# Optimization experiments

Measured on AMD Instinct MI355X. Metric: run time of the kernel, lower is better.

Reference implementation:

```python
import jax, jax.numpy as jnp
import numpy as np

B, T, H, NH = 2, 2048, 2048, 16
HD = H // NH  # 128


def setup_inputs() -> dict:
    key = jax.random.key(0)
    ks = jax.random.split(key, 7)
    s = 1.0 / np.sqrt(H)
    return {
        "x": jax.random.normal(ks[0], (B, T, H), jnp.float32),
        "cos": jax.random.uniform(ks[1], (1, 1, T, HD), jnp.float32),
        "sin": jax.random.uniform(ks[2], (1, 1, T, HD), jnp.float32),
        "Wq": jax.random.normal(ks[3], (H, H), jnp.float32) * s,
        "Wk": jax.random.normal(ks[4], (H, H), jnp.float32) * s,
        "Wv": jax.random.normal(ks[5], (H, H), jnp.float32) * s,
        "Wo": jax.random.normal(ks[6], (H, H), jnp.float32) * s,
    }


def rotate_half(x):
    d = x.shape[-1] // 2
    return jnp.concatenate([-x[..., d:], x[..., :d]], axis=-1)


def reference(x, cos, sin, Wq, Wk, Wv, Wo):
    b, t, h = x.shape
    # torch Linear: y = x @ W.T; reshape to (B, NH, T, HD)
    def proj(W):
        return jnp.einsum('bth,oh->bto', x, W).reshape(b, t, NH, HD).transpose(0, 2, 1, 3)
    q, k, v = proj(Wq), proj(Wk), proj(Wv)
    q = q * cos + rotate_half(q) * sin
    k = k * cos + rotate_half(k) * sin
    scale = 1.0 / jnp.sqrt(jnp.asarray(HD, x.dtype))
    scores = jnp.einsum('bhqd,bhkd->bhqk', q, k) * scale  # [B,NH,T,T]
    causal = jnp.tril(jnp.ones((t, t), bool))
    scores = jnp.where(causal, scores, jnp.asarray(-jnp.inf, scores.dtype))
    attn = jax.nn.softmax(scores, axis=-1)
    out = jnp.einsum('bhqk,bhkd->bhqd', attn, v)  # [B,NH,T,HD]
    out = out.transpose(0, 2, 1, 3).reshape(b, t, h)
    return jnp.einsum('bth,oh->bto', out, Wo)
```

## Files before the change

### kernel.cpp

```cpp
#include <hip/hip_runtime.h>
#include <hip/hip_bf16.h>

#define B_  2
#define T_  2048
#define H_  2048
#define NH_ 16
#define HD_ 128
#define QKVN 6144

typedef __attribute__((ext_vector_type(8))) short  short8;
typedef __attribute__((ext_vector_type(4))) float  floatx4;

__device__ __forceinline__ unsigned short f2bf(float x) {
    union { float f; unsigned int u; } c; c.f = x;
    unsigned int r = c.u + 0x7FFF + ((c.u >> 16) & 1);
    return (unsigned short)(r >> 16);
}
__device__ __forceinline__ float bf2f(unsigned short u) {
    union { float f; unsigned int i; } c;
    c.i = ((unsigned int)u) << 16;
    return c.f;
}

__device__ __forceinline__ void gload_lds16(const void* g, void* l) {
    __builtin_amdgcn_global_load_lds(
        (__attribute__((address_space(1))) void*)g,
        (__attribute__((address_space(3))) void*)l, 16, 0, 0);
}

__global__ __launch_bounds__(256) void f32_to_bf16(
    const float* __restrict__ src, unsigned short* __restrict__ dst, int n)
{
    const int i = (blockIdx.x * 256 + threadIdx.x) * 4;
    if (i < n) {
        float4 v = *(const float4*)(src + i);
        ushort4 o;
        o.x = f2bf(v.x); o.y = f2bf(v.y); o.z = f2bf(v.z); o.w = f2bf(v.w);
        *(ushort4*)(dst + i) = o;
    }
}

template<bool BF16_OUT>
__global__ __launch_bounds__(512, 1) void gemm8(
    const unsigned short* __restrict__ A,
    const unsigned short* __restrict__ W,
    float* __restrict__ Yf, unsigned short* __restrict__ Yb,
    int M, int N, int K)
{
    __shared__ __attribute__((aligned(16))) unsigned short As[2][256 * 64];
    __shared__ __attribute__((aligned(16))) unsigned short Bs[2][256 * 64];

    const int tid  = threadIdx.x;
    const int lane = tid & 63;
    const int n16  = lane & 15;
    const int quad = lane >> 4;
    const int w    = tid >> 6;
    const int wm   = w >> 2;
    const int wn   = w & 3;

    const int m0 = blockIdx.y * 256;
    const int n0 = blockIdx.x * 256;

    const int r0  = tid >> 3;
    const int g0  = ((tid & 7) ^ (r0 & 7)) * 8;
    const int r1  = r0 + 64;
    const int g1  = ((tid & 7) ^ (r1 & 7)) * 8;
    const unsigned short* A0p = A + (size_t)(m0 + r0) * K + g0;
    const unsigned short* A1p = A + (size_t)(m0 + r1) * K + g1;
    const unsigned short* B0p = W + (size_t)(n0 + r0) * K + g0;
    const unsigned short* B1p = W + (size_t)(n0 + r1) * K + g1;
    const size_t hstep = (size_t)128 * K;

    floatx4 acc[8][4];
    #pragma unroll
    for (int i = 0; i < 8; i++)
        #pragma unroll
        for (int j = 0; j < 4; j++) acc[i][j] = (floatx4){0.f, 0.f, 0.f, 0.f};

    const int nt = K >> 6;

    gload_lds16(A0p,         &As[0][(size_t)tid * 8]);
    gload_lds16(A1p,         &As[0][(size_t)(tid + 512) * 8]);
    gload_lds16(A0p + hstep, &As[0][8192 + (size_t)tid * 8]);
    gload_lds16(A1p + hstep, &As[0][8192 + (size_t)(tid + 512) * 8]);
    gload_lds16(B0p,         &Bs[0][(size_t)tid * 8]);
    gload_lds16(B1p,         &Bs[0][(size_t)(tid + 512) * 8]);
    gload_lds16(B0p + hstep, &Bs[0][8192 + (size_t)tid * 8]);
    gload_lds16(B1p + hstep, &Bs[0][8192 + (size_t)(tid + 512) * 8]);

    for (int t = 0; t < nt; ++t) {
        const unsigned short* Ac = &As[t & 1][0];
        const unsigned short* Bc = &Bs[t & 1][0];
        unsigned short* An = &As[(t & 1) ^ 1][0];
        unsigned short* Bn = &Bs[(t & 1) ^ 1][0];
        const bool pre = (t + 1 < nt);
        const size_t knext = (size_t)(t + 1) << 6;

        short8 bfr[4][2];

        #pragma unroll
        for (int q = 0; q < 4; ++q) {
            short8 af[2][2];
            if (q == 0) {
                if (pre) {
                    gload_lds16(A0p + knext,         An + (size_t)tid * 8);
                    gload_lds16(A1p + knext,         An + (size_t)(tid + 512) * 8);
                    gload_lds16(A0p + knext + hstep, An + 8192 + (size_t)tid * 8);
                    gload_lds16(A1p + knext + hstep, An + 8192 + (size_t)(tid + 512) * 8);
                    asm volatile("s_waitcnt vmcnt(4)" ::: "memory");
                } else {
                    asm volatile("s_waitcnt vmcnt(0)" ::: "memory");
                }
                asm volatile("s_barrier" ::: "memory");
                #pragma unroll
                for (int j = 0; j < 2; ++j)
                    #pragma unroll
                    for (int ks = 0; ks < 2; ++ks)
                        af[j][ks] = *(const short8*)(Ac + (wm*128 + (q*2 + j)*16 + n16) * 64
                                                        + (((ks*4 + quad) ^ (n16 & 7)) * 8));
                #pragma unroll
                for (int ni = 0; ni < 4; ++ni)
                    #pragma unroll
                    for (int ks = 0; ks < 2; ++ks)
                        bfr[ni][ks] = *(const short8*)(Bc + (wn*64 + ni*16 + n16) * 64
                                                          + (((ks*4 + quad) ^ (n16 & 7)) * 8));
            } else {
                #pragma unroll
                for (int j = 0; j < 2; ++j)
                    #pragma unroll
                    for (int ks = 0; ks < 2; ++ks)
                        af[j][ks] = *(const short8*)(Ac + (wm*128 + (q*2 + j)*16 + n16) * 64
                                                        + (((ks*4 + quad) ^ (n16 & 7)) * 8));
                if (q == 1 && pre) {
                    gload_lds16(B0p + knext,         Bn + (size_t)tid * 8);
                    gload_lds16(B1p + knext,         Bn + (size_t)(tid + 512) * 8);
                    gload_lds16(B0p + knext + hstep, Bn + 8192 + (size_t)tid * 8);
                    gload_lds16(B1p + knext + hstep, Bn + 8192 + (size_t)(tid + 512) * 8);
                }
                asm volatile("s_barrier" ::: "memory");
            }
            asm volatile("s_waitcnt lgkmcnt(0)" ::: "memory");
            __builtin_amdgcn_sched_barrier(0);
            __builtin_amdgcn_s_setprio(1);
            #pragma unroll
            for (int ni = 0; ni < 4; ++ni)
                #pragma unroll
                for (int ks = 0; ks < 2; ++ks) {
                    acc[q*2+0][ni] = __builtin_amdgcn_mfma_f32_16x16x32_bf16(
                        af[0][ks], bfr[ni][ks], acc[q*2+0][ni], 0, 0, 0);
                    acc[q*2+1][ni] = __builtin_amdgcn_mfma_f32_16x16x32_bf16(
                        af[1][ks], bfr[ni][ks], acc[q*2+1][ni], 0, 0, 0);
                }
            __builtin_amdgcn_s_setprio(0);
            asm volatile("s_barrier" ::: "memory");
        }
    }

    #pragma unroll
    for (int mi = 0; mi < 8; ++mi) {
        const size_t rb = (size_t)(m0 + wm*128 + mi*16 + quad*4);
        #pragma unroll
        for (int r = 0; r < 4; ++r) {
            const size_t row = rb + r;
            #pragma unroll
            for (int ni = 0; ni < 4; ++ni) {
                const size_t col = n0 + wn*64 + ni*16 + n16;
                if (BF16_OUT) Yb[row * N + col] = f2bf(acc[mi][ni][r]);
                else          Yf[row * N + col] = acc[mi][ni][r];
            }
        }
    }
}

__global__ __launch_bounds__(256) void rope_convert_qk(
    const unsigned short* __restrict__ qkvp,
    const float* __restrict__ cosp, const float* __restrict__ sinp,
    unsigned short* __restrict__ qh, unsigned short* __restrict__ kh)
{
    const int idx  = blockIdx.x * 256 + threadIdx.x;
    const int d    = idx & 63;
    const int rest = idx >> 6;
    const int h    = rest & 15;
    const int bt   = rest >> 4;
    const int t    = bt & (T_ - 1);
    const int b    = bt >> 11;
    const size_t ibase = (size_t)bt * QKVN + h * HD_;
    const size_t obase = (((size_t)b * NH_ + h) * T_ + t) * HD_;

    const float c0 = cosp[t*HD_ + d],      s0 = sinp[t*HD_ + d];
    const float c1 = cosp[t*HD_ + d + 64], s1 = sinp[t*HD_ + d + 64];
    const float sc = 0.08838834764831845f;

    float q0 = bf2f(qkvp[ibase + d]), q1 = bf2f(qkvp[ibase + d + 64]);
    qh[obase + d]      = f2bf((q0*c0 - q1*s0) * sc);
    qh[obase + d + 64] = f2bf((q1*c1 + q0*s1) * sc);

    float k0 = bf2f(qkvp[ibase + 2048 + d]), k1 = bf2f(qkvp[ibase + 2048 + d + 64]);
    kh[obase + d]      = f2bf(k0*c0 - k1*s0);
    kh[obase + d + 64] = f2bf(k1*c1 + k0*s1);
}

__global__ __launch_bounds__(256) void transpose_v(
    const unsigned short* __restrict__ qkvp, unsigned short* __restrict__ vh)
{
    __shared__ float tile[64][65];
    const int t0 = blockIdx.x * 64;
    const int d0 = blockIdx.y * 64;
    const int bh = blockIdx.z;
    const int b  = bh >> 4, h = bh & 15;

    for (int i = threadIdx.x; i < 4096; i += 256) {
        int r = i >> 6, c = i & 63;
        tile[r][c] = bf2f(qkvp[((size_t)b*T_ + t0 + r) * QKVN + 4096 + h*HD_ + d0 + c]);
    }
    __syncthreads();
    for (int i = threadIdx.x; i < 4096; i += 256) {
        int dr = i >> 6, tc = i & 63;
        vh[((size_t)bh * HD_ + d0 + dr) * T_ + t0 + tc] = f2bf(tile[tc][dr]);
    }
}

__global__ __launch_bounds__(256, 4) void attn_mfma(
    const unsigned short* __restrict__ qh,
    const unsigned short* __restrict__ kh,
    const unsigned short* __restrict__ vh,
    unsigned short* __restrict__ o)
{
    __shared__ __attribute__((aligned(16))) unsigned short Ks[64 * 128];
    __shared__ __attribute__((aligned(16))) unsigned short Vs[128 * 64];
    __shared__ __attribute__((aligned(16))) unsigned short Ps[4][16 * 64];

    const int tid  = threadIdx.x;
    const int lane = tid & 63;
    const int w    = tid >> 6;
    const int n16  = lane & 15;
    const int quad = lane >> 4;

    const int id   = blockIdx.y * gridDim.x + blockIdx.x;
    const int bh   = id & 31;
    const int a    = (id >> 5) & 7;
    const int u    = id >> 8;
    const int qblk = (u < 2) ? (a + (u << 3)) : ((23 + ((u & 1) << 3)) - a);

    const int q0w  = qblk * 64 + w * 16;

    short8 qf[4];
    {
        const size_t qbase = ((size_t)bh * T_ + q0w + n16) * HD_ + quad * 8;
        #pragma unroll
        for (int c = 0; c < 4; c++)
            qf[c] = *(const short8*)(qh + qbase + c * 32);
    }

    const int rk   = tid >> 4;
    const int gk16 = ((tid & 15) ^ (rk & 7)) * 8;
    const unsigned short* ksrc = kh + (size_t)bh * T_ * HD_ + (size_t)rk * HD_ + gk16;
    const int dv   = tid >> 3;
    const int gv16 = ((tid & 7) ^ (dv & 7)) * 8;
    const unsigned short* vsrc = vh + (size_t)bh * HD_ * T_ + (size_t)dv * T_ + gv16;

    floatx4 of[8];
    #pragma unroll
    for (int i = 0; i < 8; i++) of[i] = (floatx4){0.f, 0.f, 0.f, 0.f};
    float mrow[4], lrow[4];
    #pragma unroll
    for (int r = 0; r < 4; r++) { mrow[r] = -INFINITY; lrow[r] = 0.f; }

    const int nkv = qblk + 1;
    for (int kv = 0; kv < nkv; kv++) {
        const int kv0 = kv * 64;
        __syncthreads();
        #pragma unroll
        for (int it = 0; it < 4; it++)
            gload_lds16(ksrc + (size_t)(kv0 + it * 16) * HD_,
                        Ks + (size_t)(it * 256 + tid) * 8);
        #pragma unroll
        for (int it = 0; it < 4; it++)
            gload_lds16(vsrc + kv0 + (size_t)(it * 32) * T_,
                        Vs + (size_t)(it * 256 + tid) * 8);
        __syncthreads();

        floatx4 s[4];
        #pragma unroll
        for (int kg = 0; kg < 4; kg++) {
            floatx4 acc = {0.f, 0.f, 0.f, 0.f};
            #pragma unroll
            for (int c = 0; c < 4; c++) {
                short8 kf = *(const short8*)(Ks + (kg*16 + n16) * 128
                                                + (((c*4 + quad) ^ (n16 & 7)) * 8));
                acc = __builtin_amdgcn_mfma_f32_16x16x32_bf16(qf[c], kf, acc, 0, 0, 0);
            }
            s[kg] = acc;
        }

        const bool needmask = (kv0 + 63 > q0w);

        float alpha[4];
        #pragma unroll
        for (int r = 0; r < 4; r++) {
            const int qrow = q0w + quad * 4 + r;
            float v0 = s[0][r], v1 = s[1][r], v2 = s[2][r], v3 = s[3][r];
            if (needmask) {
                if (kv0 +  0 + n16 > qrow) v0 = -INFINITY;
                if (kv0 + 16 + n16 > qrow) v1 = -INFINITY;
                if (kv0 + 32 + n16 > qrow) v2 = -INFINITY;
                if (kv0 + 48 + n16 > qrow) v3 = -INFINITY;
            }

            float tm = fmaxf(fmaxf(v0, v1), fmaxf(v2, v3));
            tm = fmaxf(tm, __shfl_xor(tm, 1));
            tm = fmaxf(tm, __shfl_xor(tm, 2));
            tm = fmaxf(tm, __shfl_xor(tm, 4));
            tm = fmaxf(tm, __shfl_xor(tm, 8));

            const float mnew = fmaxf(mrow[r], tm);
            const float aa   = __expf(mrow[r] - mnew);
            const float p0 = __expf(v0 - mnew), p1 = __expf(v1 - mnew);
            const float p2 = __expf(v2 - mnew), p3 = __expf(v3 - mnew);

            float ts = p0 + p1 + p2 + p3;
            ts += __shfl_xor(ts, 1);
            ts += __shfl_xor(ts, 2);
            ts += __shfl_xor(ts, 4);
            ts += __shfl_xor(ts, 8);

            lrow[r] = lrow[r] * aa + ts;
            mrow[r] = mnew;
            alpha[r] = aa;

            const int pr = quad * 4 + r;
            const int sx = pr & 7;
            unsigned short* pp = &Ps[w][pr * 64];
            const int g0p = n16 >> 3, e = n16 & 7;
            pp[((g0p    ) ^ sx) * 8 + e] = f2bf(p0);
            pp[((g0p + 2) ^ sx) * 8 + e] = f2bf(p1);
            pp[((g0p + 4) ^ sx) * 8 + e] = f2bf(p2);
            pp[((g0p + 6) ^ sx) * 8 + e] = f2bf(p3);
        }
        #pragma unroll
        for (int nt = 0; nt < 8; nt++)
            #pragma unroll
            for (int r = 0; r < 4; r++) of[nt][r] *= alpha[r];

        short8 pf0 = *(const short8*)(&Ps[w][n16 * 64 + ((quad       ^ (n16 & 7)) * 8)]);
        short8 pf1 = *(const short8*)(&Ps[w][n16 * 64 + (((quad + 4) ^ (n16 & 7)) * 8)]);
        #pragma unroll
        for (int nt = 0; nt < 8; nt++) {
            const int vr = (nt * 16 + n16) * 64;
            short8 vf0 = *(const short8*)(Vs + vr + ((quad       ^ (n16 & 7)) * 8));
            short8 vf1 = *(const short8*)(Vs + vr + (((quad + 4) ^ (n16 & 7)) * 8));
            of[nt] = __builtin_amdgcn_mfma_f32_16x16x32_bf16(pf0, vf0, of[nt], 0, 0, 0);
            of[nt] = __builtin_amdgcn_mfma_f32_16x16x32_bf16(pf1, vf1, of[nt], 0, 0, 0);
        }
    }

    const int b = bh >> 4, h = bh & 15;
    #pragma unroll
    for (int r = 0; r < 4; r++) {
        const float inv = 1.f / lrow[r];
        const size_t orow = ((size_t)b * T_ + q0w + quad*4 + r) * H_ + h * HD_;
        #pragma unroll
        for (int nt = 0; nt < 8; nt++)
            o[orow + nt*16 + n16] = f2bf(of[nt][r] * inv);
    }
}

extern "C" void kernel_launch(void* const* d_in, const int* in_sizes, int n_in,
                              void* d_out, int out_size, void* d_ws, size_t ws_size,
                              hipStream_t stream)
{
    const float* x    = (const float*)d_in[0];
    const float* cosp = (const float*)d_in[1];
    const float* sinp = (const float*)d_in[2];
    const float* Wq   = (const float*)d_in[3];
    const float* Wk   = (const float*)d_in[4];
    const float* Wv   = (const float*)d_in[5];
    const float* Wo   = (const float*)d_in[6];

    const size_t NEL  = (size_t)B_ * T_ * H_;
    const int    XN   = (int)NEL;
    const int    WN   = H_ * H_;
    char* ws = (char*)d_ws;
    const size_t MB16 = 16777216;

    unsigned short* xh    = (unsigned short*)(ws);
    unsigned short* Wqkvh = (unsigned short*)(ws + MB16);
    unsigned short* Woh   = (unsigned short*)(ws + MB16*5/2);
    unsigned short* qkvp  = (unsigned short*)(ws + 3*MB16);
    unsigned short* kh    = (unsigned short*)(ws + 6*MB16);
    unsigned short* qh    = (unsigned short*)(ws + MB16);
    unsigned short* vh    = (unsigned short*)(ws);
    unsigned short* abh   = (unsigned short*)(ws + 3*MB16);

    f32_to_bf16<<<XN/1024, 256, 0, stream>>>(x,  xh,  XN);
    f32_to_bf16<<<WN/1024, 256, 0, stream>>>(Wq, Wqkvh,          WN);
    f32_to_bf16<<<WN/1024, 256, 0, stream>>>(Wk, Wqkvh +   WN,   WN);
    f32_to_bf16<<<WN/1024, 256, 0, stream>>>(Wv, Wqkvh + 2*WN,   WN);
    f32_to_bf16<<<WN/1024, 256, 0, stream>>>(Wo, Woh,            WN);

    const int M = B_ * T_;

    gemm8<true><<<dim3(QKVN/256, M/256), 512, 0, stream>>>(xh, Wqkvh, nullptr, qkvp, M, QKVN, H_);

    rope_convert_qk<<<(B_*T_*NH_*64)/256, 256, 0, stream>>>(qkvp, cosp, sinp, qh, kh);
    transpose_v<<<dim3(T_/64, HD_/64, B_*NH_), 256, 0, stream>>>(qkvp, vh);

    attn_mfma<<<dim3(T_/64, B_*NH_), 256, 0, stream>>>(qh, kh, vh, abh);

    gemm8<false><<<dim3(H_/256, M/256), 512, 0, stream>>>(abh, Woh, (float*)d_out, nullptr, M, H_, H_);
}
```

Before: 489.1 us.

## Software-pipeline LDS fragment loads with MFMA and remap GEMM blocks across XCDs

Restructures the bf16 GEMM main loop so A-fragment LDS reads for the next quarter-step are issued before the MFMAs of the current one, using ping-pong register fragments and a loop unrolled by two over the LDS double buffers. Prefetches of both A and B for the next K tile are issued together at the start of each tile. Block IDs are remapped so consecutive tiles land on the same XCD, aiming to improve L2 reuse. This raises register pressure, and the reworked waitcnt/barrier placement must stay correct, for example when nt is odd.

```diff
diff --git a/kernel.cpp b/kernel.cpp
--- a/kernel.cpp
+++ b/kernel.cpp
@@ -38,6 +38,107 @@
         o.x = f2bf(v.x); o.y = f2bf(v.y); o.z = f2bf(v.z); o.w = f2bf(v.w);
         *(ushort4*)(dst + i) = o;
     }
+}
+
+template<int QQ>
+__device__ __forceinline__ void ld_af(short8 (&d)[2][2], const unsigned short* src,
+                                      int wm, int n16, int quad)
+{
+    #pragma unroll
+    for (int j = 0; j < 2; ++j)
+        #pragma unroll
+        for (int ks = 0; ks < 2; ++ks)
+            d[j][ks] = *(const short8*)(src + (wm*128 + (QQ*2 + j)*16 + n16) * 64
+                                            + (((ks*4 + quad) ^ (n16 & 7)) * 8));
+}
+
+__device__ __forceinline__ void ld_bfr(short8 (&d)[4][2], const unsigned short* src,
+                                       int wn, int n16, int quad)
+{
+    #pragma unroll
+    for (int ni = 0; ni < 4; ++ni)
+        #pragma unroll
+        for (int ks = 0; ks < 2; ++ks)
+            d[ni][ks] = *(const short8*)(src + (wn*64 + ni*16 + n16) * 64
+                                             + (((ks*4 + quad) ^ (n16 & 7)) * 8));
+}
+
+template<int QQ>
+__device__ __forceinline__ void mfma_quad(floatx4 (&acc)[8][4],
+                                          const short8 (&af)[2][2],
+                                          const short8 (&bf)[4][2])
+{
+    #pragma unroll
+    for (int ni = 0; ni < 4; ++ni)
+        #pragma unroll
+        for (int ks = 0; ks < 2; ++ks) {
+            acc[QQ*2+0][ni] = __builtin_amdgcn_mfma_f32_16x16x32_bf16(
+                af[0][ks], bf[ni][ks], acc[QQ*2+0][ni], 0, 0, 0);
+            acc[QQ*2+1][ni] = __builtin_amdgcn_mfma_f32_16x16x32_bf16(
+                af[1][ks], bf[ni][ks], acc[QQ*2+1][ni], 0, 0, 0);
+        }
+}
+
+__device__ __forceinline__ void g8_tile(
+    const unsigned short* Ac, const unsigned short* Bc,
+    unsigned short* An, unsigned short* Bn,
+    const unsigned short* A0p, const unsigned short* A1p,
+    const unsigned short* B0p, const unsigned short* B1p,
+    size_t hstep, size_t knext, bool pre, int tid,
+    int wm, int wn, int n16, int quad,
+    short8 (&afA)[2][2], short8 (&afB)[2][2], short8 (&bfr)[4][2],
+    floatx4 (&acc)[8][4])
+{
+    if (pre) {
+        gload_lds16(A0p + knext,         An + (size_t)tid * 8);
+        gload_lds16(A1p + knext,         An + (size_t)(tid + 512) * 8);
+        gload_lds16(A0p + knext + hstep, An + 8192 + (size_t)tid * 8);
+        gload_lds16(A1p + knext + hstep, An + 8192 + (size_t)(tid + 512) * 8);
+        gload_lds16(B0p + knext,         Bn + (size_t)tid * 8);
+        gload_lds16(B1p + knext,         Bn + (size_t)(tid + 512) * 8);
+        gload_lds16(B0p + knext + hstep, Bn + 8192 + (size_t)tid * 8);
+        gload_lds16(B1p + knext + hstep, Bn + 8192 + (size_t)(tid + 512) * 8);
+    }
+    ld_af<1>(afB, Ac, wm, n16, quad);
+    asm volatile("s_barrier" ::: "memory");
+    asm volatile("s_waitcnt lgkmcnt(4)" ::: "memory");
+    __builtin_amdgcn_sched_barrier(0);
+    ld_bfr(bfr, Bc, wn, n16, quad);
+    asm volatile("s_waitcnt lgkmcnt(0)" ::: "memory");
+    __builtin_amdgcn_sched_barrier(0);
+    __builtin_amdgcn_s_setprio(1);
+    mfma_quad<0>(acc, afA, bfr);
+    __builtin_amdgcn_s_setprio(0);
+    asm volatile("s_barrier" ::: "memory");
+
+    ld_af<2>(afA, Ac, wm, n16, quad);
+    asm volatile("s_barrier" ::: "memory");
+    asm volatile("s_waitcnt lgkmcnt(4)" ::: "memory");
+    __builtin_amdgcn_sched_barrier(0);
+    __builtin_amdgcn_s_setprio(1);
+    mfma_quad<1>(acc, afB, bfr);
+    __builtin_amdgcn_s_setprio(0);
+    asm volatile("s_barrier" ::: "memory");
+
+    ld_af<3>(afB, Ac, wm, n16, quad);
+    asm volatile("s_barrier" ::: "memory");
+    asm volatile("s_waitcnt lgkmcnt(4)" ::: "memory");
+    __builtin_amdgcn_sched_barrier(0);
+    __builtin_amdgcn_s_setprio(1);
+    mfma_quad<2>(acc, afA, bfr);
+    __builtin_amdgcn_s_setprio(0);
+    asm volatile("s_waitcnt vmcnt(0)" ::: "memory");
+    asm volatile("s_barrier" ::: "memory");
+
+    if (pre) ld_af<0>(afA, An, wm, n16, quad);
+    asm volatile("s_barrier" ::: "memory");
+    if (pre) asm volatile("s_waitcnt lgkmcnt(4)" ::: "memory");
+    else     asm volatile("s_waitcnt lgkmcnt(0)" ::: "memory");
+    __builtin_amdgcn_sched_barrier(0);
+    __builtin_amdgcn_s_setprio(1);
+    mfma_quad<3>(acc, afB, bfr);
+    __builtin_amdgcn_s_setprio(0);
+    asm volatile("s_barrier" ::: "memory");
 }
 
 template<bool BF16_OUT>
@@ -58,17 +159,19 @@
     const int wm   = w >> 2;
     const int wn   = w & 3;
 
-    const int m0 = blockIdx.y * 256;
-    const int n0 = blockIdx.x * 256;
+    const int gx   = gridDim.x;
+    const int id   = blockIdx.y * gx + blockIdx.x;
+    const int cpx  = (gx * gridDim.y) >> 3;
+    const int nid  = (id & 7) * cpx + (id >> 3);
+    const int m0   = (nid / gx) * 256;
+    const int n0   = (nid % gx) * 256;
 
     const int r0  = tid >> 3;
     const int g0  = ((tid & 7) ^ (r0 & 7)) * 8;
-    const int r1  = r0 + 64;
-    const int g1  = ((tid & 7) ^ (r1 & 7)) * 8;
     const unsigned short* A0p = A + (size_t)(m0 + r0) * K + g0;
-    const unsigned short* A1p = A + (size_t)(m0 + r1) * K + g1;
+    const unsigned short* A1p = A + (size_t)(m0 + 64 + r0) * K + g0;
     const unsigned short* B0p = W + (size_t)(n0 + r0) * K + g0;
-    const unsigned short* B1p = W + (size_t)(n0 + r1) * K + g1;
+    const unsigned short* B1p = W + (size_t)(n0 + 64 + r0) * K + g0;
     const size_t hstep = (size_t)128 * K;
 
     floatx4 acc[8][4];
@@ -88,72 +191,21 @@
     gload_lds16(B0p + hstep, &Bs[0][8192 + (size_t)tid * 8]);
     gload_lds16(B1p + hstep, &Bs[0][8192 + (size_t)(tid + 512) * 8]);
 
-    for (int t = 0; t < nt; ++t) {
-        const unsigned short* Ac = &As[t & 1][0];
-        const unsigned short* Bc = &Bs[t & 1][0];
-        unsigned short* An = &As[(t & 1) ^ 1][0];
-        unsigned short* Bn = &Bs[(t & 1) ^ 1][0];
-        const bool pre = (t + 1 < nt);
-        const size_t knext = (size_t)(t + 1) << 6;
-
-        short8 bfr[4][2];
-
-        #pragma unroll
-        for (int q = 0; q < 4; ++q) {
-            short8 af[2][2];
-            if (q == 0) {
-                if (pre) {
-                    gload_lds16(A0p + knext,         An + (size_t)tid * 8);
-                    gload_lds16(A1p + knext,         An + (size_t)(tid + 512) * 8);
-                    gload_lds16(A0p + knext + hstep, An + 8192 + (size_t)tid * 8);
-                    gload_lds16(A1p + knext + hstep, An + 8192 + (size_t)(tid + 512) * 8);
-                    asm volatile("s_waitcnt vmcnt(4)" ::: "memory");
-                } else {
-                    asm volatile("s_waitcnt vmcnt(0)" ::: "memory");
-                }
-                asm volatile("s_barrier" ::: "memory");
-                #pragma unroll
-                for (int j = 0; j < 2; ++j)
-                    #pragma unroll
-                    for (int ks = 0; ks < 2; ++ks)
-                        af[j][ks] = *(const short8*)(Ac + (wm*128 + (q*2 + j)*16 + n16) * 64
-                                                        + (((ks*4 + quad) ^ (n16 & 7)) * 8));
-                #pragma unroll
-                for (int ni = 0; ni < 4; ++ni)
-                    #pragma unroll
-                    for (int ks = 0; ks < 2; ++ks)
-                        bfr[ni][ks] = *(const short8*)(Bc + (wn*64 + ni*16 + n16) * 64
-                                                          + (((ks*4 + quad) ^ (n16 & 7)) * 8));
-            } else {
-                #pragma unroll
-                for (int j = 0; j < 2; ++j)
-                    #pragma unroll
-                    for (int ks = 0; ks < 2; ++ks)
-                        af[j][ks] = *(const short8*)(Ac + (wm*128 + (q*2 + j)*16 + n16) * 64
-                                                        + (((ks*4 + quad) ^ (n16 & 7)) * 8));
-                if (q == 1 && pre) {
-                    gload_lds16(B0p + knext,         Bn + (size_t)tid * 8);
-                    gload_lds16(B1p + knext,         Bn + (size_t)(tid + 512) * 8);
-                    gload_lds16(B0p + knext + hstep, Bn + 8192 + (size_t)tid * 8);
-                    gload_lds16(B1p + knext + hstep, Bn + 8192 + (size_t)(tid + 512) * 8);
-                }
-                asm volatile("s_barrier" ::: "memory");
-            }
-            asm volatile("s_waitcnt lgkmcnt(0)" ::: "memory");
-            __builtin_amdgcn_sched_barrier(0);
-            __builtin_amdgcn_s_setprio(1);
-            #pragma unroll
-            for (int ni = 0; ni < 4; ++ni)
-                #pragma unroll
-                for (int ks = 0; ks < 2; ++ks) {
-                    acc[q*2+0][ni] = __builtin_amdgcn_mfma_f32_16x16x32_bf16(
-                        af[0][ks], bfr[ni][ks], acc[q*2+0][ni], 0, 0, 0);
-                    acc[q*2+1][ni] = __builtin_amdgcn_mfma_f32_16x16x32_bf16(
-                        af[1][ks], bfr[ni][ks], acc[q*2+1][ni], 0, 0, 0);
-                }
-            __builtin_amdgcn_s_setprio(0);
-            asm volatile("s_barrier" ::: "memory");
-        }
+    short8 afA[2][2], afB[2][2], bfr[4][2];
+
+    asm volatile("s_waitcnt vmcnt(0)" ::: "memory");
+    asm volatile("s_barrier" ::: "memory");
+    ld_af<0>(afA, &As[0][0], wm, n16, quad);
+
+    for (int t = 0; t < nt; t += 2) {
+        g8_tile(&As[0][0], &Bs[0][0], &As[1][0], &Bs[1][0],
+                A0p, A1p, B0p, B1p, hstep,
+                (size_t)(t + 1) << 6, (t + 1) < nt,
+                tid, wm, wn, n16, quad, afA, afB, bfr, acc);
+        g8_tile(&As[1][0], &Bs[1][0], &As[0][0], &Bs[0][0],
+                A0p, A1p, B0p, B1p, hstep,
+                (size_t)(t + 2) << 6, (t + 2) < nt,
+                tid, wm, wn, n16, quad, afA, afB, bfr, acc);
     }
 
     #pragma unroll
```

New measurement: 477.8 us. 1.02x faster.

## Restructure GEMM main loop into 4 quadrant phases with reuse of A/B fragments

Applied to the files above, without the earlier changes.

Each K-tile is now split into four 128x32-per-wave quadrants, and A and B register fragments are reused across two quadrants each. Before, every step reloaded A fragments and B was loaded once for all four steps. The change also moves the whole-tile vmcnt wait to the end of the iteration, before the last quadrant, so global-to-LDS prefetch of the next tile overlaps more of the compute. The aim is fewer LDS reads and better overlap of memory with MFMA, at the cost of more live registers and more barriers per iteration.

```diff
diff --git a/kernel.cpp b/kernel.cpp
--- a/kernel.cpp
+++ b/kernel.cpp
@@ -39,6 +39,47 @@
         *(ushort4*)(dst + i) = o;
     }
 }
+
+template<int MB>
+__device__ __forceinline__ void ld_a4(short8 (&d)[4][2], const unsigned short* src,
+                                      int wm, int n16, int quad)
+{
+    #pragma unroll
+    for (int mi = 0; mi < 4; ++mi)
+        #pragma unroll
+        for (int ks = 0; ks < 2; ++ks)
+            d[mi][ks] = *(const short8*)(src + (wm*128 + (MB+mi)*16 + n16) * 64
+                                             + (((ks*4 + quad) ^ (n16 & 7)) * 8));
+}
+template<int NB>
+__device__ __forceinline__ void ld_b2(short8 (&d)[2][2], const unsigned short* src,
+                                      int wn, int n16, int quad)
+{
+    #pragma unroll
+    for (int ni = 0; ni < 2; ++ni)
+        #pragma unroll
+        for (int ks = 0; ks < 2; ++ks)
+            d[ni][ks] = *(const short8*)(src + (wn*64 + (NB+ni)*16 + n16) * 64
+                                             + (((ks*4 + quad) ^ (n16 & 7)) * 8));
+}
+template<int MB, int NB>
+__device__ __forceinline__ void mfma_q(floatx4 (&acc)[8][4],
+                                       const short8 (&a)[4][2],
+                                       const short8 (&b)[2][2])
+{
+    #pragma unroll
+    for (int ks = 0; ks < 2; ++ks)
+        #pragma unroll
+        for (int mi = 0; mi < 4; ++mi)
+            #pragma unroll
+            for (int ni = 0; ni < 2; ++ni)
+                acc[MB+mi][NB+ni] = __builtin_amdgcn_mfma_f32_16x16x32_bf16(
+                    a[mi][ks], b[ni][ks], acc[MB+mi][NB+ni], 0, 0, 0);
+}
+
+#define BAR()  asm volatile("s_barrier" ::: "memory")
+#define LGKM0() do { asm volatile("s_waitcnt lgkmcnt(0)" ::: "memory"); \
+                     __builtin_amdgcn_sched_barrier(0); } while (0)
 
 template<bool BF16_OUT>
 __global__ __launch_bounds__(512, 1) void gemm8(
@@ -63,12 +104,10 @@
 
     const int r0  = tid >> 3;
     const int g0  = ((tid & 7) ^ (r0 & 7)) * 8;
-    const int r1  = r0 + 64;
-    const int g1  = ((tid & 7) ^ (r1 & 7)) * 8;
     const unsigned short* A0p = A + (size_t)(m0 + r0) * K + g0;
-    const unsigned short* A1p = A + (size_t)(m0 + r1) * K + g1;
+    const unsigned short* A1p = A + (size_t)(m0 + 64 + r0) * K + g0;
     const unsigned short* B0p = W + (size_t)(n0 + r0) * K + g0;
-    const unsigned short* B1p = W + (size_t)(n0 + r1) * K + g1;
+    const unsigned short* B1p = W + (size_t)(n0 + 64 + r0) * K + g0;
     const size_t hstep = (size_t)128 * K;
 
     floatx4 acc[8][4];
@@ -87,6 +126,8 @@
     gload_lds16(B1p,         &Bs[0][(size_t)(tid + 512) * 8]);
     gload_lds16(B0p + hstep, &Bs[0][8192 + (size_t)tid * 8]);
     gload_lds16(B1p + hstep, &Bs[0][8192 + (size_t)(tid + 512) * 8]);
+    asm volatile("s_waitcnt vmcnt(0)" ::: "memory");
+    BAR();
 
     for (int t = 0; t < nt; ++t) {
         const unsigned short* Ac = &As[t & 1][0];
@@ -96,64 +137,53 @@
         const bool pre = (t + 1 < nt);
         const size_t knext = (size_t)(t + 1) << 6;
 
-        short8 bfr[4][2];
-
-        #pragma unroll
-        for (int q = 0; q < 4; ++q) {
-            short8 af[2][2];
-            if (q == 0) {
-                if (pre) {
-                    gload_lds16(A0p + knext,         An + (size_t)tid * 8);
-                    gload_lds16(A1p + knext,         An + (size_t)(tid + 512) * 8);
-                    gload_lds16(A0p + knext + hstep, An + 8192 + (size_t)tid * 8);
-                    gload_lds16(A1p + knext + hstep, An + 8192 + (size_t)(tid + 512) * 8);
-                    asm volatile("s_waitcnt vmcnt(4)" ::: "memory");
-                } else {
-                    asm volatile("s_waitcnt vmcnt(0)" ::: "memory");
-                }
-                asm volatile("s_barrier" ::: "memory");
-                #pragma unroll
-                for (int j = 0; j < 2; ++j)
-                    #pragma unroll
-                    for (int ks = 0; ks < 2; ++ks)
-                        af[j][ks] = *(const short8*)(Ac + (wm*128 + (q*2 + j)*16 + n16) * 64
-                                                        + (((ks*4 + quad) ^ (n16 & 7)) * 8));
-                #pragma unroll
-                for (int ni = 0; ni < 4; ++ni)
-                    #pragma unroll
-                    for (int ks = 0; ks < 2; ++ks)
-                        bfr[ni][ks] = *(const short8*)(Bc + (wn*64 + ni*16 + n16) * 64
-                                                          + (((ks*4 + quad) ^ (n16 & 7)) * 8));
-            } else {
-                #pragma unroll
-                for (int j = 0; j < 2; ++j)
-                    #pragma unroll
-                    for (int ks = 0; ks < 2; ++ks)
-                        af[j][ks] = *(const short8*)(Ac + (wm*128 + (q*2 + j)*16 + n16) * 64
-                                                        + (((ks*4 + quad) ^ (n16 & 7)) * 8));
-                if (q == 1 && pre) {
-                    gload_lds16(B0p + knext,         Bn + (size_t)tid * 8);
-                    gload_lds16(B1p + knext,         Bn + (size_t)(tid + 512) * 8);
-                    gload_lds16(B0p + knext + hstep, Bn + 8192 + (size_t)tid * 8);
-                    gload_lds16(B1p + knext + hstep, Bn + 8192 + (size_t)(tid + 512) * 8);
-                }
-                asm volatile("s_barrier" ::: "memory");
-            }
-            asm volatile("s_waitcnt lgkmcnt(0)" ::: "memory");
-            __builtin_amdgcn_sched_barrier(0);
-            __builtin_amdgcn_s_setprio(1);
-            #pragma unroll
-            for (int ni = 0; ni < 4; ++ni)
-                #pragma unroll
-                for (int ks = 0; ks < 2; ++ks) {
-                    acc[q*2+0][ni] = __builtin_amdgcn_mfma_f32_16x16x32_bf16(
-                        af[0][ks], bfr[ni][ks], acc[q*2+0][ni], 0, 0, 0);
-                    acc[q*2+1][ni] = __builtin_amdgcn_mfma_f32_16x16x32_bf16(
-                        af[1][ks], bfr[ni][ks], acc[q*2+1][ni], 0, 0, 0);
-                }
-            __builtin_amdgcn_s_setprio(0);
-            asm volatile("s_barrier" ::: "memory");
-        }
+        short8 afL[4][2], afH[4][2], bfL[2][2], bfH[2][2];
+
+        ld_a4<0>(afL, Ac, wm, n16, quad);
+        ld_b2<0>(bfL, Bc, wn, n16, quad);
+        if (pre) {
+            gload_lds16(A0p + knext,         An + (size_t)tid * 8);
+            gload_lds16(A1p + knext,         An + (size_t)(tid + 512) * 8);
+            gload_lds16(A0p + knext + hstep, An + 8192 + (size_t)tid * 8);
+            gload_lds16(A1p + knext + hstep, An + 8192 + (size_t)(tid + 512) * 8);
+        }
+        asm volatile("s_waitcnt lgkmcnt(8)" ::: "memory");
+        BAR();
+        LGKM0();
+        __builtin_amdgcn_s_setprio(1);
+        mfma_q<0, 0>(acc, afL, bfL);
+        __builtin_amdgcn_s_setprio(0);
+        BAR();
+
+        ld_b2<2>(bfH, Bc, wn, n16, quad);
+        if (pre) {
+            gload_lds16(B0p + knext,         Bn + (size_t)tid * 8);
+            gload_lds16(B1p + knext,         Bn + (size_t)(tid + 512) * 8);
+            gload_lds16(B0p + knext + hstep, Bn + 8192 + (size_t)tid * 8);
+            gload_lds16(B1p + knext + hstep, Bn + 8192 + (size_t)(tid + 512) * 8);
+        }
+        BAR();
+        LGKM0();
+        __builtin_amdgcn_s_setprio(1);
+        mfma_q<0, 2>(acc, afL, bfH);
+        __builtin_amdgcn_s_setprio(0);
+        BAR();
+
+        ld_a4<4>(afH, Ac, wm, n16, quad);
+        BAR();
+        LGKM0();
+        __builtin_amdgcn_s_setprio(1);
+        mfma_q<4, 0>(acc, afH, bfL);
+        __builtin_amdgcn_s_setprio(0);
+        BAR();
+
+        asm volatile("s_waitcnt vmcnt(0)" ::: "memory");
+        BAR();
+        __builtin_amdgcn_sched_barrier(0);
+        __builtin_amdgcn_s_setprio(1);
+        mfma_q<4, 2>(acc, afH, bfH);
+        __builtin_amdgcn_s_setprio(0);
+        BAR();
     }
 
     #pragma unroll
```

After: 451.1 us. 1.08x faster.
